# Kernel optimization log

Measured on AMD Instinct MI355X. Metric: run time of the kernel, lower is better.

Reference implementation:

```python
import jax, jax.numpy as jnp
import numpy as np

N = 50000      # nodes
E = 800000     # edges (before self-loops)
F_IN = 32      # num_node_features
H = 4          # heads
C = 64         # per-head channels (graph_hidden_channels // nheads)
HID = H * C    # 256
G = 1024       # number of graphs in batch
MLP_HID = 2048
NOUT = 768
NEG_SLOPE = 0.2


def setup_inputs() -> dict:
    key = jax.random.key(0)
    ks = jax.random.split(key, 24)
    def nrm(k, shape, s=0.05):
        return jax.random.normal(k, shape, jnp.float32) * s
    x = jax.random.normal(ks[0], (N, F_IN), jnp.float32)
    edge_index = jax.random.randint(ks[1], (2, E), 0, N)
    batch = jnp.sort(jax.random.randint(ks[2], (N,), 0, G))
    return {
        'x': x, 'edge_index': edge_index, 'batch': batch,
        'W1': nrm(ks[3], (F_IN, HID)), 'a_src1': nrm(ks[4], (H, C)), 'a_dst1': nrm(ks[5], (H, C)), 'b1': jnp.zeros((HID,), jnp.float32),
        'W2': nrm(ks[6], (HID, HID)), 'a_src2': nrm(ks[7], (H, C)), 'a_dst2': nrm(ks[8], (H, C)), 'b2': jnp.zeros((HID,), jnp.float32),
        'W3': nrm(ks[9], (HID, HID)), 'a_src3': nrm(ks[10], (H, C)), 'a_dst3': nrm(ks[11], (H, C)), 'b3': jnp.zeros((HID,), jnp.float32),
        'Wm1': nrm(ks[12], (HID, MLP_HID)), 'bm1': jnp.zeros((MLP_HID,), jnp.float32),
        'Wm2': nrm(ks[13], (MLP_HID, NOUT)), 'bm2': jnp.zeros((NOUT,), jnp.float32),
        'gamma': jnp.ones((NOUT,), jnp.float32), 'beta': jnp.zeros((NOUT,), jnp.float32),
    }


def _gat_layer(x, src, dst, W, a_s, a_d, b):
    # PyG GATConv (eval mode, dropout inactive), self-loops already in src/dst.
    h = (x @ W).reshape(N, H, C)                       # [N,H,C]
    ls = (h * a_s).sum(-1)                             # [N,H] source att logits
    ld = (h * a_d).sum(-1)                             # [N,H] target att logits
    logits = jax.nn.leaky_relu(ls[src] + ld[dst], NEG_SLOPE)  # [E',H]
    m = jax.ops.segment_max(logits, dst, num_segments=N)
    m = jnp.where(jnp.isfinite(m), m, 0.0)
    e = jnp.exp(logits - m[dst])
    denom = jax.ops.segment_sum(e, dst, num_segments=N) + 1e-16
    alpha = e / denom[dst]                             # segment softmax per dst node
    out = jax.ops.segment_sum(h[src] * alpha[:, :, None], dst, num_segments=N)
    return out.reshape(N, HID) + b


def reference(x, edge_index, batch, W1, a_src1, a_dst1, b1, W2, a_src2, a_dst2, b2,
              W3, a_src3, a_dst3, b3, Wm1, bm1, Wm2, bm2, gamma, beta):
    loop = jnp.arange(N)
    src = jnp.concatenate([edge_index[0], loop])
    dst = jnp.concatenate([edge_index[1], loop])
    h = jax.nn.relu(_gat_layer(x, src, dst, W1, a_src1, a_dst1, b1))
    h = jax.nn.relu(_gat_layer(h, src, dst, W2, a_src2, a_dst2, b2))
    h = _gat_layer(h, src, dst, W3, a_src3, a_dst3, b3)
    # global_mean_pool
    sums = jax.ops.segment_sum(h, batch, num_segments=G)
    counts = jax.ops.segment_sum(jnp.ones((N, 1), jnp.float32), batch, num_segments=G)
    pooled = sums / jnp.maximum(counts, 1.0)           # [G,HID]
    z = jax.nn.relu(pooled @ Wm1 + bm1)
    z = z @ Wm2 + bm2
    mu = z.mean(-1, keepdims=True)
    var = z.var(-1, keepdims=True)
    return gamma * (z - mu) * jax.lax.rsqrt(var + 1e-5) + beta
```

## Files before the change

kernel.cpp:

```cpp
#include <hip/hip_runtime.h>
#include <math.h>

#define N_NODES 50000
#define N_EDGES 800000
#define N_ETOT  850000
#define F_IN    32
#define HEADS   4
#define CHAN    64
#define HID     256
#define NGRAPH  1024
#define MLP_HID 2048
#define NOUT    768
#define NEG_SLOPE 0.2f
#define KSPL    4
#define NBLK    ((N_NODES + 255) / 256)

typedef __attribute__((ext_vector_type(8))) short short8v;
typedef __attribute__((ext_vector_type(4))) float f32x4;

__device__ __forceinline__ unsigned short f2bf(float f) {
    unsigned u = __float_as_uint(f);
    u += 0x7fff + ((u >> 16) & 1);
    return (unsigned short)(u >> 16);
}
__device__ __forceinline__ float bf2f(unsigned short s) {
    return __uint_as_float((unsigned)s << 16);
}

__global__ __launch_bounds__(256) void hist_kernel(const int* __restrict__ ei,
                                                   int* __restrict__ deg) {
    int e = blockIdx.x * 256 + threadIdx.x;
    if (e >= N_ETOT) return;
    int d = (e < N_EDGES) ? ei[N_EDGES + e] : (e - N_EDGES);
    atomicAdd(&deg[d], 1);
}

__global__ __launch_bounds__(256) void bsum_kernel(const int* __restrict__ deg,
                                                   int* __restrict__ bsum) {
    const int t = threadIdx.x;
    int i = blockIdx.x * 256 + t;
    int v = (i < N_NODES) ? deg[i] : 0;
    #pragma unroll
    for (int o = 32; o > 0; o >>= 1) v += __shfl_down(v, o);
    __shared__ int red[4];
    if ((t & 63) == 0) red[t >> 6] = v;
    __syncthreads();
    if (t == 0) bsum[blockIdx.x] = red[0] + red[1] + red[2] + red[3];
}

__global__ __launch_bounds__(256) void bscan_kernel(const int* __restrict__ bsum,
                                                    int* __restrict__ bpre,
                                                    int* __restrict__ off) {
    __shared__ int s[256];
    const int t = threadIdx.x;
    int v = (t < NBLK) ? bsum[t] : 0;
    s[t] = v;
    __syncthreads();
    for (int d = 1; d < 256; d <<= 1) {
        int u = (t >= d) ? s[t - d] : 0;
        __syncthreads();
        s[t] += u;
        __syncthreads();
    }
    if (t < NBLK) bpre[t] = s[t] - v;
    if (t == NBLK - 1) off[N_NODES] = s[t];
}

__global__ __launch_bounds__(256) void cscan_kernel(const int* __restrict__ deg,
                                                    const int* __restrict__ bpre,
                                                    int* __restrict__ off,
                                                    int* __restrict__ cur) {
    __shared__ int s[256];
    const int t = threadIdx.x;
    const int i = blockIdx.x * 256 + t;
    int v = (i < N_NODES) ? deg[i] : 0;
    s[t] = v;
    __syncthreads();
    for (int d = 1; d < 256; d <<= 1) {
        int u = (t >= d) ? s[t - d] : 0;
        __syncthreads();
        s[t] += u;
        __syncthreads();
    }
    if (i < N_NODES) {
        int pre = bpre[blockIdx.x] + s[t] - v;
        off[i] = pre;
        cur[i] = pre;
    }
}

__global__ __launch_bounds__(256) void scatter_kernel(const int* __restrict__ ei,
                                                      int* __restrict__ cur,
                                                      int* __restrict__ ssrc) {
    int e = blockIdx.x * 256 + threadIdx.x;
    if (e >= N_ETOT) return;
    int s, d;
    if (e < N_EDGES) { s = ei[e]; d = ei[N_EDGES + e]; }
    else             { s = e - N_EDGES; d = s; }
    int pos = atomicAdd(&cur[d], 1);
    ssrc[pos] = s;
}

__global__ __launch_bounds__(256) void castT_kernel(const float* __restrict__ W,
                                                    unsigned short* __restrict__ Wt) {
    const int r = blockIdx.x;
    const int c = threadIdx.x;
    Wt[(size_t)c * HID + r] = f2bf(W[(size_t)r * HID + c]);
}

__global__ __launch_bounds__(256) void gemm_mfma_bt(const float* __restrict__ A,
                                                    const unsigned short* __restrict__ Bt,
                                                    float* __restrict__ C,
                                                    int M) {
    __shared__ unsigned short Asb[64][32];
    __shared__ unsigned short Bsb[64][32];
    const int t = threadIdx.x;
    const int wave = t >> 6;
    const int lane = t & 63;
    const int bm = blockIdx.x * 64;
    const int bn = blockIdx.y * 64;
    const int sr = t >> 2;
    const int skq = (t & 3) * 8;
    const int fr = lane & 15;
    const int fq = lane >> 4;

    f32x4 acc[4] = {{0.f,0.f,0.f,0.f},{0.f,0.f,0.f,0.f},
                    {0.f,0.f,0.f,0.f},{0.f,0.f,0.f,0.f}};

    for (int k0 = 0; k0 < HID; k0 += 32) {
        {
            const int gr = bm + sr;
            float4 v0 = make_float4(0.f,0.f,0.f,0.f), v1 = v0;
            if (gr < M) {
                v0 = *(const float4*)&A[(size_t)gr * HID + k0 + skq];
                v1 = *(const float4*)&A[(size_t)gr * HID + k0 + skq + 4];
            }
            ushort4 q0, q1;
            q0.x = f2bf(v0.x); q0.y = f2bf(v0.y); q0.z = f2bf(v0.z); q0.w = f2bf(v0.w);
            q1.x = f2bf(v1.x); q1.y = f2bf(v1.y); q1.z = f2bf(v1.z); q1.w = f2bf(v1.w);
            *(ushort4*)&Asb[sr][skq]     = q0;
            *(ushort4*)&Asb[sr][skq + 4] = q1;
        }
        *(short8v*)&Bsb[sr][skq] =
            *(const short8v*)&Bt[(size_t)(bn + sr) * HID + k0 + skq];
        __syncthreads();

        short8v a = *(short8v*)&Asb[wave * 16 + fr][fq * 8];
        #pragma unroll
        for (int nt = 0; nt < 4; ++nt) {
            short8v b = *(short8v*)&Bsb[nt * 16 + fr][fq * 8];
            acc[nt] = __builtin_amdgcn_mfma_f32_16x16x32_bf16(a, b, acc[nt], 0, 0, 0);
        }
        __syncthreads();
    }

    #pragma unroll
    for (int nt = 0; nt < 4; ++nt) {
        #pragma unroll
        for (int r = 0; r < 4; ++r) {
            int row = bm + wave * 16 + fq * 4 + r;
            if (row < M)
                C[(size_t)row * HID + bn + nt * 16 + fr] = acc[nt][r];
        }
    }
}

template <int BM, int BN, int TM, int TN, bool BIAS, bool RELU, bool SPLITK>
__global__ __launch_bounds__(256) void gemm_kernel(const float* __restrict__ A,
                                                   const float* __restrict__ B,
                                                   const float* __restrict__ bias,
                                                   float* __restrict__ C,
                                                   int M, int Nn, int K, int lda) {
    __shared__ float As[16][BM + 4];
    __shared__ float Bs[16][BN + 4];
    if (SPLITK) {
        const int z = blockIdx.z;
        A += (size_t)z * K;
        B += (size_t)z * K * Nn;
        C += (size_t)z * M * Nn;
    }
    const int t = threadIdx.x;
    const int bm = blockIdx.x * BM;
    const int bn = blockIdx.y * BN;
    constexpr int NTX = BN / TN;
    const int tx = t % NTX;
    const int ty = t / NTX;
    const int row0 = ty * TM;
    const int col0 = tx * TN;
    constexpr int BN4 = BN / 4;
    constexpr int AITER = BM * 4 / 256;
    constexpr int BITER = 16 * BN4 / 256;

    float acc[TM][TN] = {};
    for (int k0 = 0; k0 < K; k0 += 16) {
        #pragma unroll
        for (int it = 0; it < AITER; ++it) {
            int f = t + it * 256;
            int m = f >> 2, kq = (f & 3) << 2;
            int gr = bm + m;
            float4 v = make_float4(0.f, 0.f, 0.f, 0.f);
            if (gr < M) v = *(const float4*)&A[(size_t)gr * lda + k0 + kq];
            As[kq + 0][m] = v.x;
            As[kq + 1][m] = v.y;
            As[kq + 2][m] = v.z;
            As[kq + 3][m] = v.w;
        }
        #pragma unroll
        for (int it = 0; it < BITER; ++it) {
            int f = t + it * 256;
            int k = f / BN4, n = (f % BN4) << 2;
            *(float4*)&Bs[k][n] = *(const float4*)&B[(size_t)(k0 + k) * Nn + bn + n];
        }
        __syncthreads();
        #pragma unroll
        for (int k = 0; k < 16; ++k) {
            float a[TM], b[TN];
            #pragma unroll
            for (int i = 0; i < TM; i += 4)
                *(float4*)&a[i] = *(const float4*)&As[k][row0 + i];
            #pragma unroll
            for (int j = 0; j < TN; j += 4)
                *(float4*)&b[j] = *(const float4*)&Bs[k][col0 + j];
            #pragma unroll
            for (int i = 0; i < TM; ++i)
                #pragma unroll
                for (int j = 0; j < TN; ++j)
                    acc[i][j] += a[i] * b[j];
        }
        __syncthreads();
    }
    #pragma unroll
    for (int i = 0; i < TM; ++i) {
        int r = bm + row0 + i;
        if (r >= M) continue;
        #pragma unroll
        for (int j = 0; j < TN; j += 4) {
            int c = bn + col0 + j;
            float4 v;
            v.x = acc[i][j + 0];
            v.y = acc[i][j + 1];
            v.z = acc[i][j + 2];
            v.w = acc[i][j + 3];
            if (BIAS) {
                const float4 bv = *(const float4*)&bias[c];
                v.x += bv.x; v.y += bv.y; v.z += bv.z; v.w += bv.w;
            }
            if (RELU) {
                v.x = fmaxf(v.x, 0.f); v.y = fmaxf(v.y, 0.f);
                v.z = fmaxf(v.z, 0.f); v.w = fmaxf(v.w, 0.f);
            }
            *(float4*)&C[(size_t)r * Nn + c] = v;
        }
    }
}

__global__ __launch_bounds__(256) void logits_kernel(const float* __restrict__ h,
                                                     const float* __restrict__ a_s,
                                                     const float* __restrict__ a_d,
                                                     float* __restrict__ ls,
                                                     float* __restrict__ ld,
                                                     unsigned short* __restrict__ hb) {
    const int lane = threadIdx.x & 63;
    const int wid  = threadIdx.x >> 6;
    const int node = blockIdx.x * 4 + wid;
    if (node >= N_NODES) return;
    const int myh = lane >> 4;

    float4 v = *(const float4*)&h[(size_t)node * HID + lane * 4];
    ushort4 q;
    q.x = f2bf(v.x); q.y = f2bf(v.y); q.z = f2bf(v.z); q.w = f2bf(v.w);
    *(ushort4*)&hb[(size_t)node * HID + lane * 4] = q;

    const float4 as4 = *(const float4*)&a_s[lane * 4];
    const float4 ad4 = *(const float4*)&a_d[lane * 4];
    float ss = v.x * as4.x + v.y * as4.y + v.z * as4.z + v.w * as4.w;
    float dd = v.x * ad4.x + v.y * ad4.y + v.z * ad4.z + v.w * ad4.w;
    #pragma unroll
    for (int o = 1; o < 16; o <<= 1) {
        ss += __shfl_xor(ss, o);
        dd += __shfl_xor(dd, o);
    }
    if ((lane & 15) == 0) {
        ls[node * HEADS + myh] = ss;
        ld[node * HEADS + myh] = dd;
    }
}

__device__ __forceinline__ float leaky(float x) { return fmaxf(x, NEG_SLOPE * x); }

template <bool RELU>
__global__ __launch_bounds__(256) void gat_aggregate(const unsigned short* __restrict__ hb,
                                                     const int* __restrict__ off,
                                                     const int* __restrict__ ssrc,
                                                     const float* __restrict__ ls,
                                                     const float* __restrict__ ld,
                                                     const float* __restrict__ bias,
                                                     float* __restrict__ h_out) {
    const int lane = threadIdx.x & 63;
    const int wid  = threadIdx.x >> 6;
    const int node = blockIdx.x * 4 + wid;
    if (node >= N_NODES) return;
    const int lo = off[node], hi = off[node + 1];
    const int myh = lane >> 4;
    const float ldv = ld[node * HEADS + myh];

    float4 acc = make_float4(0.f, 0.f, 0.f, 0.f);
    float den = 0.f;
    int e = lo;
    for (; e + 2 <= hi; e += 2) {
        int s0 = ssrc[e];
        int s1 = ssrc[e + 1];
        float l0 = ls[s0 * HEADS + myh];
        float l1 = ls[s1 * HEADS + myh];
        ushort4 q0 = *(const ushort4*)&hb[(size_t)s0 * HID + lane * 4];
        ushort4 q1 = *(const ushort4*)&hb[(size_t)s1 * HID + lane * 4];
        float w0 = __expf(leaky(l0 + ldv));
        float w1 = __expf(leaky(l1 + ldv));
        den += w0 + w1;
        acc.x += w0 * bf2f(q0.x) + w1 * bf2f(q1.x);
        acc.y += w0 * bf2f(q0.y) + w1 * bf2f(q1.y);
        acc.z += w0 * bf2f(q0.z) + w1 * bf2f(q1.z);
        acc.w += w0 * bf2f(q0.w) + w1 * bf2f(q1.w);
    }
    if (e < hi) {
        int s0 = ssrc[e];
        float w0 = __expf(leaky(ls[s0 * HEADS + myh] + ldv));
        ushort4 q0 = *(const ushort4*)&hb[(size_t)s0 * HID + lane * 4];
        den += w0;
        acc.x += w0 * bf2f(q0.x); acc.y += w0 * bf2f(q0.y);
        acc.z += w0 * bf2f(q0.z); acc.w += w0 * bf2f(q0.w);
    }
    float inv = 1.f / (den + 1e-16f);
    float4 bv = *(const float4*)(bias + lane * 4);
    float4 o;
    o.x = acc.x * inv + bv.x; o.y = acc.y * inv + bv.y;
    o.z = acc.z * inv + bv.z; o.w = acc.w * inv + bv.w;
    if (RELU) {
        o.x = fmaxf(o.x, 0.f); o.y = fmaxf(o.y, 0.f);
        o.z = fmaxf(o.z, 0.f); o.w = fmaxf(o.w, 0.f);
    }
    *(float4*)(h_out + (size_t)node * HID + lane * 4) = o;
}

__global__ __launch_bounds__(256) void pool_kernel(const float* __restrict__ h,
                                                   const int* __restrict__ batch,
                                                   float* __restrict__ pooled) {
    const int g = blockIdx.x;
    __shared__ int bounds[2];
    if (threadIdx.x < 2) {
        int target = g + threadIdx.x;
        int lo = 0, hi = N_NODES;
        while (lo < hi) {
            int mid = (lo + hi) >> 1;
            if (batch[mid] < target) lo = mid + 1; else hi = mid;
        }
        bounds[threadIdx.x] = lo;
    }
    __syncthreads();
    const int lo = bounds[0], hi = bounds[1];
    const int c = threadIdx.x;
    float s = 0.f;
    for (int i = lo; i < hi; ++i) s += h[(size_t)i * HID + c];
    float cnt = (float)max(hi - lo, 1);
    pooled[(size_t)g * HID + c] = s / cnt;
}

__global__ __launch_bounds__(256) void ln_kernel(const float* __restrict__ z2p,
                                                 const float* __restrict__ bm2,
                                                 const float* __restrict__ gamma,
                                                 const float* __restrict__ beta,
                                                 float* __restrict__ out) {
    const int row = blockIdx.x;
    float v[3];
    float s = 0.f, s2 = 0.f;
    #pragma unroll
    for (int i = 0; i < 3; ++i) {
        int c = threadIdx.x + i * 256;
        float a = bm2[c];
        #pragma unroll
        for (int sp = 0; sp < KSPL; ++sp)
            a += z2p[(size_t)sp * NGRAPH * NOUT + (size_t)row * NOUT + c];
        v[i] = a;
        s += a;
        s2 += a * a;
    }
    #pragma unroll
    for (int o = 32; o > 0; o >>= 1) {
        s  += __shfl_down(s, o);
        s2 += __shfl_down(s2, o);
    }
    __shared__ float red[8];
    const int wid = threadIdx.x >> 6, lane = threadIdx.x & 63;
    if (lane == 0) { red[wid] = s; red[4 + wid] = s2; }
    __syncthreads();
    if (threadIdx.x == 0) {
        float S  = red[0] + red[1] + red[2] + red[3];
        float S2 = red[4] + red[5] + red[6] + red[7];
        float mu  = S / NOUT;
        float var = S2 / NOUT - mu * mu;
        red[0] = mu;
        red[1] = rsqrtf(var + 1e-5f);
    }
    __syncthreads();
    float mu = red[0], rstd = red[1];
    #pragma unroll
    for (int i = 0; i < 3; ++i) {
        int c = threadIdx.x + i * 256;
        out[(size_t)row * NOUT + c] = gamma[c] * (v[i] - mu) * rstd + beta[c];
    }
}

extern "C" void kernel_launch(void* const* d_in, const int* in_sizes, int n_in,
                              void* d_out, int out_size, void* d_ws, size_t ws_size,
                              hipStream_t stream) {
    const float* x     = (const float*)d_in[0];
    const int*   ei    = (const int*)d_in[1];
    const int*   batch = (const int*)d_in[2];
    const float* W1    = (const float*)d_in[3];
    const float* a_s1  = (const float*)d_in[4];
    const float* a_d1  = (const float*)d_in[5];
    const float* b1    = (const float*)d_in[6];
    const float* W2    = (const float*)d_in[7];
    const float* a_s2  = (const float*)d_in[8];
    const float* a_d2  = (const float*)d_in[9];
    const float* b2    = (const float*)d_in[10];
    const float* W3    = (const float*)d_in[11];
    const float* a_s3  = (const float*)d_in[12];
    const float* a_d3  = (const float*)d_in[13];
    const float* b3    = (const float*)d_in[14];
    const float* Wm1   = (const float*)d_in[15];
    const float* bm1   = (const float*)d_in[16];
    const float* Wm2   = (const float*)d_in[17];
    const float* bm2   = (const float*)d_in[18];
    const float* gamma = (const float*)d_in[19];
    const float* beta  = (const float*)d_in[20];
    float* out = (float*)d_out;

    char* p = (char*)d_ws;
    auto alloc = [&](size_t bytes) {
        void* r = (void*)p;
        p += (bytes + 255) & ~(size_t)255;
        return r;
    };
    int*   deg    = (int*)  alloc((size_t)N_NODES * 4);
    int*   off    = (int*)  alloc((size_t)(N_NODES + 1) * 4);
    int*   cur    = (int*)  alloc((size_t)N_NODES * 4);
    int*   ssrc   = (int*)  alloc((size_t)N_ETOT * 4);
    int*   bsum   = (int*)  alloc((size_t)256 * 4);
    int*   bpre   = (int*)  alloc((size_t)256 * 4);
    float* ls     = (float*)alloc((size_t)N_NODES * HEADS * 4);
    float* ld     = (float*)alloc((size_t)N_NODES * HEADS * 4);
    float* hA     = (float*)alloc((size_t)N_NODES * HID * 4);
    float* hB     = (float*)alloc((size_t)N_NODES * HID * 4);
    unsigned short* hb  = (unsigned short*)alloc((size_t)N_NODES * HID * 2);
    unsigned short* W2t = (unsigned short*)alloc((size_t)HID * HID * 2);
    unsigned short* W3t = (unsigned short*)alloc((size_t)HID * HID * 2);
    float* pooled = (float*)alloc((size_t)NGRAPH * HID * 4);
    float* z1     = (float*)alloc((size_t)NGRAPH * MLP_HID * 4);
    float* z2p    = (float*)alloc((size_t)KSPL * NGRAPH * NOUT * 4);

    hipMemsetAsync(deg, 0, (size_t)N_NODES * 4, stream);
    hist_kernel<<<(N_ETOT + 255) / 256, 256, 0, stream>>>(ei, deg);
    bsum_kernel<<<NBLK, 256, 0, stream>>>(deg, bsum);
    bscan_kernel<<<1, 256, 0, stream>>>(bsum, bpre, off);
    cscan_kernel<<<NBLK, 256, 0, stream>>>(deg, bpre, off, cur);
    scatter_kernel<<<(N_ETOT + 255) / 256, 256, 0, stream>>>(ei, cur, ssrc);
    castT_kernel<<<HID, 256, 0, stream>>>(W2, W2t);
    castT_kernel<<<HID, 256, 0, stream>>>(W3, W3t);

    const int nodeBlocks = (N_NODES + 3) / 4;
    dim3 mfmaGrid((N_NODES + 63) / 64, HID / 64);

    dim3 gemmN((N_NODES + 127) / 128, HID / 128);
    gemm_kernel<128, 128, 8, 8, false, false, false><<<gemmN, 256, 0, stream>>>(x, W1, nullptr, hA, N_NODES, HID, F_IN, F_IN);
    logits_kernel<<<nodeBlocks, 256, 0, stream>>>(hA, a_s1, a_d1, ls, ld, hb);
    gat_aggregate<true><<<nodeBlocks, 256, 0, stream>>>(hb, off, ssrc, ls, ld, b1, hB);

    gemm_mfma_bt<<<mfmaGrid, 256, 0, stream>>>(hB, W2t, hA, N_NODES);
    logits_kernel<<<nodeBlocks, 256, 0, stream>>>(hA, a_s2, a_d2, ls, ld, hb);
    gat_aggregate<true><<<nodeBlocks, 256, 0, stream>>>(hb, off, ssrc, ls, ld, b2, hB);

    gemm_mfma_bt<<<mfmaGrid, 256, 0, stream>>>(hB, W3t, hA, N_NODES);
    logits_kernel<<<nodeBlocks, 256, 0, stream>>>(hA, a_s3, a_d3, ls, ld, hb);
    gat_aggregate<false><<<nodeBlocks, 256, 0, stream>>>(hb, off, ssrc, ls, ld, b3, hB);

    pool_kernel<<<NGRAPH, 256, 0, stream>>>(hB, batch, pooled);
    dim3 gm1(NGRAPH / 64, MLP_HID / 128);
    gemm_kernel<64, 128, 4, 8, true, true, false><<<gm1, 256, 0, stream>>>(pooled, Wm1, bm1, z1, NGRAPH, MLP_HID, HID, HID);
    dim3 gm2(NGRAPH / 64, NOUT / 64, KSPL);
    gemm_kernel<64, 64, 4, 4, false, false, true><<<gm2, 256, 0, stream>>>(z1, Wm2, nullptr, z2p, NGRAPH, NOUT, MLP_HID / KSPL, MLP_HID);
    ln_kernel<<<NGRAPH, 256, 0, stream>>>(z2p, bm2, gamma, beta, out);
}
```

Measured before the change: 659.3 us.

## Fuse attention logits and bf16 cast into MFMA GEMM epilogue; unroll aggregation by 4

The MFMA GEMM for layers 2 and 3 now computes per-head source and destination attention logits in its epilogue, using a shuffle reduction across the 16 lanes covering a head's channels. It writes bf16 features directly, which removes the fp32 intermediate write and read and the separate logits kernel launch. The aggregation loop is also unrolled to four edges per iteration so more gathers are in flight. The costs are extra register pressure in both kernels and a scattered 2-byte store pattern for the bf16 output.

After: 627.8 us. 1.05x faster.

```diff
diff --git a/kernel.cpp b/kernel.cpp
--- a/kernel.cpp
+++ b/kernel.cpp
@@ -108,17 +108,22 @@
     Wt[(size_t)c * HID + r] = f2bf(W[(size_t)r * HID + c]);
 }
 
-__global__ __launch_bounds__(256) void gemm_mfma_bt(const float* __restrict__ A,
-                                                    const unsigned short* __restrict__ Bt,
-                                                    float* __restrict__ C,
-                                                    int M) {
+__global__ __launch_bounds__(256) void gemm_mfma_fused(const float* __restrict__ A,
+                                                       const unsigned short* __restrict__ Bt,
+                                                       const float* __restrict__ a_s,
+                                                       const float* __restrict__ a_d,
+                                                       unsigned short* __restrict__ hb,
+                                                       float* __restrict__ ls,
+                                                       float* __restrict__ ld,
+                                                       int M) {
     __shared__ unsigned short Asb[64][32];
     __shared__ unsigned short Bsb[64][32];
     const int t = threadIdx.x;
     const int wave = t >> 6;
     const int lane = t & 63;
     const int bm = blockIdx.x * 64;
-    const int bn = blockIdx.y * 64;
+    const int head = blockIdx.y;
+    const int bn = head * 64;
     const int sr = t >> 2;
     const int skq = (t & 3) * 8;
     const int fr = lane & 15;
@@ -154,13 +159,38 @@
         __syncthreads();
     }
 
+    float pS[4] = {0.f, 0.f, 0.f, 0.f};
+    float pD[4] = {0.f, 0.f, 0.f, 0.f};
     #pragma unroll
     for (int nt = 0; nt < 4; ++nt) {
+        const float asv = a_s[head * CHAN + nt * 16 + fr];
+        const float adv = a_d[head * CHAN + nt * 16 + fr];
+        #pragma unroll
+        for (int r = 0; r < 4; ++r) {
+            const float c = acc[nt][r];
+            pS[r] += c * asv;
+            pD[r] += c * adv;
+            int row = bm + wave * 16 + fq * 4 + r;
+            if (row < M)
+                hb[(size_t)row * HID + bn + nt * 16 + fr] = f2bf(c);
+        }
+    }
+    #pragma unroll
+    for (int o = 1; o < 16; o <<= 1) {
+        #pragma unroll
+        for (int r = 0; r < 4; ++r) {
+            pS[r] += __shfl_xor(pS[r], o);
+            pD[r] += __shfl_xor(pD[r], o);
+        }
+    }
+    if (fr == 0) {
         #pragma unroll
         for (int r = 0; r < 4; ++r) {
             int row = bm + wave * 16 + fq * 4 + r;
-            if (row < M)
-                C[(size_t)row * HID + bn + nt * 16 + fr] = acc[nt][r];
+            if (row < M) {
+                ls[row * HEADS + head] = pS[r];
+                ld[row * HEADS + head] = pD[r];
+            }
         }
     }
 }
@@ -307,22 +337,24 @@
     float4 acc = make_float4(0.f, 0.f, 0.f, 0.f);
     float den = 0.f;
     int e = lo;
-    for (; e + 2 <= hi; e += 2) {
-        int s0 = ssrc[e];
-        int s1 = ssrc[e + 1];
-        float l0 = ls[s0 * HEADS + myh];
-        float l1 = ls[s1 * HEADS + myh];
+    for (; e + 4 <= hi; e += 4) {
+        int s0 = ssrc[e],     s1 = ssrc[e + 1];
+        int s2 = ssrc[e + 2], s3 = ssrc[e + 3];
+        float l0 = ls[s0 * HEADS + myh], l1 = ls[s1 * HEADS + myh];
+        float l2 = ls[s2 * HEADS + myh], l3 = ls[s3 * HEADS + myh];
         ushort4 q0 = *(const ushort4*)&hb[(size_t)s0 * HID + lane * 4];
         ushort4 q1 = *(const ushort4*)&hb[(size_t)s1 * HID + lane * 4];
-        float w0 = __expf(leaky(l0 + ldv));
-        float w1 = __expf(leaky(l1 + ldv));
-        den += w0 + w1;
-        acc.x += w0 * bf2f(q0.x) + w1 * bf2f(q1.x);
-        acc.y += w0 * bf2f(q0.y) + w1 * bf2f(q1.y);
-        acc.z += w0 * bf2f(q0.z) + w1 * bf2f(q1.z);
-        acc.w += w0 * bf2f(q0.w) + w1 * bf2f(q1.w);
-    }
-    if (e < hi) {
+        ushort4 q2 = *(const ushort4*)&hb[(size_t)s2 * HID + lane * 4];
+        ushort4 q3 = *(const ushort4*)&hb[(size_t)s3 * HID + lane * 4];
+        float w0 = __expf(leaky(l0 + ldv)), w1 = __expf(leaky(l1 + ldv));
+        float w2 = __expf(leaky(l2 + ldv)), w3 = __expf(leaky(l3 + ldv));
+        den += (w0 + w1) + (w2 + w3);
+        acc.x += w0 * bf2f(q0.x) + w1 * bf2f(q1.x) + w2 * bf2f(q2.x) + w3 * bf2f(q3.x);
+        acc.y += w0 * bf2f(q0.y) + w1 * bf2f(q1.y) + w2 * bf2f(q2.y) + w3 * bf2f(q3.y);
+        acc.z += w0 * bf2f(q0.z) + w1 * bf2f(q1.z) + w2 * bf2f(q2.z) + w3 * bf2f(q3.z);
+        acc.w += w0 * bf2f(q0.w) + w1 * bf2f(q1.w) + w2 * bf2f(q2.w) + w3 * bf2f(q3.w);
+    }
+    for (; e < hi; ++e) {
         int s0 = ssrc[e];
         float w0 = __expf(leaky(ls[s0 * HEADS + myh] + ldv));
         ushort4 q0 = *(const ushort4*)&hb[(size_t)s0 * HID + lane * 4];
@@ -469,19 +501,17 @@
     castT_kernel<<<HID, 256, 0, stream>>>(W3, W3t);
 
     const int nodeBlocks = (N_NODES + 3) / 4;
-    dim3 mfmaGrid((N_NODES + 63) / 64, HID / 64);
+    dim3 mfmaGrid((N_NODES + 63) / 64, HEADS);
 
     dim3 gemmN((N_NODES + 127) / 128, HID / 128);
     gemm_kernel<128, 128, 8, 8, false, false, false><<<gemmN, 256, 0, stream>>>(x, W1, nullptr, hA, N_NODES, HID, F_IN, F_IN);
     logits_kernel<<<nodeBlocks, 256, 0, stream>>>(hA, a_s1, a_d1, ls, ld, hb);
     gat_aggregate<true><<<nodeBlocks, 256, 0, stream>>>(hb, off, ssrc, ls, ld, b1, hB);
 
-    gemm_mfma_bt<<<mfmaGrid, 256, 0, stream>>>(hB, W2t, hA, N_NODES);
-    logits_kernel<<<nodeBlocks, 256, 0, stream>>>(hA, a_s2, a_d2, ls, ld, hb);
+    gemm_mfma_fused<<<mfmaGrid, 256, 0, stream>>>(hB, W2t, a_s2, a_d2, hb, ls, ld, N_NODES);
     gat_aggregate<true><<<nodeBlocks, 256, 0, stream>>>(hb, off, ssrc, ls, ld, b2, hB);
 
-    gemm_mfma_bt<<<mfmaGrid, 256, 0, stream>>>(hB, W3t, hA, N_NODES);
-    logits_kernel<<<nodeBlocks, 256, 0, stream>>>(hA, a_s3, a_d3, ls, ld, hb);
+    gemm_mfma_fused<<<mfmaGrid, 256, 0, stream>>>(hB, W3t, a_s3, a_d3, hb, ls, ld, N_NODES);
     gat_aggregate<false><<<nodeBlocks, 256, 0, stream>>>(hb, off, ssrc, ls, ld, b3, hB);
 
     pool_kernel<<<NGRAPH, 256, 0, stream>>>(hB, batch, pooled);
```
